# Performance work log

Hardware: AMD Instinct MI355X
Metric: run time of the kernel (lower is better)

The kernel has to match this reference:

```python
import jax, jax.numpy as jnp
import numpy as np

B, NF, S, L, H, MID, KS, NC, DENSE = 16, 8, 16, 256, 128, 32, 8, 10, 512
COEFF = 0.1
BN_EPS = 1e-5


def _normalize(x):
    return x / jnp.maximum(jnp.linalg.norm(x, axis=-1, keepdims=True), 1e-12)


def _sparsemax(z):
    # sparsemax over last axis (Martins & Astudillo 2016)
    zs = jnp.flip(jnp.sort(z, axis=-1), axis=-1)
    k = jnp.arange(1, z.shape[-1] + 1, dtype=z.dtype)
    cum = jnp.cumsum(zs, axis=-1)
    support = (1.0 + k * zs) > cum
    ksup = jnp.sum(support, axis=-1, keepdims=True)
    tau = (jnp.take_along_axis(cum, ksup - 1, axis=-1) - 1.0) / ksup.astype(z.dtype)
    return jnp.maximum(z - tau, 0.0)


def _bn_ncl(x, g, b, m, v):  # eval-mode BatchNorm1d on [N, C, L]
    return g[None, :, None] * (x - m[None, :, None]) * jax.lax.rsqrt(v[None, :, None] + BN_EPS) + b[None, :, None]


def _bn_nc(x, g, b, m, v):  # eval-mode BatchNorm1d on [N, C]
    return g * (x - m) * jax.lax.rsqrt(v + BN_EPS) + b


def _conv(x, w, pad):
    return jax.lax.conv_general_dilated(x, w, (1,), [(pad, pad)], dimension_numbers=('NCH', 'OIH', 'NCH'))


def _maxpool2(x):  # MaxPool1d(kernel=2, stride=2, padding=1): -inf padded
    return jax.lax.reduce_window(x, -jnp.inf, jax.lax.max, (1, 1, 2), (1, 1, 2), ((0, 0), (0, 0), (1, 1)))


def _cnn(x, cw1, bn1, cw2, bn2, cw3, bn3):
    x = _maxpool2(jax.nn.relu(_bn_ncl(_conv(x, cw1, KS // 2), *bn1)))
    x = _maxpool2(jax.nn.relu(_bn_ncl(_conv(x, cw2, 4), *bn2)))
    x = _maxpool2(jax.nn.relu(_bn_ncl(_conv(x, cw3, 4), *bn3)))
    return jnp.mean(x, axis=-1)  # AdaptiveAvgPool1d(1) -> [N, H]


def _alpha_beta(x, cw1, bn1, cw2, bn2, cw3, bn3, Wq, bq, Wk, bk, Wv, bv):
    b = x.shape[0]
    xf = jnp.transpose(x, (1, 0, 2, 3)).reshape(NF, b * S, 1, L)
    rep = jax.vmap(_cnn)(xf, cw1, bn1, cw2, bn2, cw3, bn3)  # [F, B*S, H]
    rep = rep.reshape(NF, b, S, H)
    Q = jax.nn.elu(rep @ Wq + bq)
    K = jax.nn.leaky_relu(rep @ Wk + bk)
    V = jax.nn.leaky_relu(rep @ Wv + bv)
    # mean_t(Q @ K^T) == Q @ mean_t(K); then scale by sqrt(d_k)
    scores = jnp.einsum('fbsh,fbh->fbs', Q, jnp.mean(K, axis=2)) / jnp.sqrt(jnp.float32(H))
    intra_aw = _sparsemax(scores)                             # [F, B, S]
    Z = _normalize(jnp.einsum('fbs,fbsh->fbh', intra_aw, V))  # [F, B, H]
    Kn = _normalize(rep)
    inter_scores = jnp.einsum('ibh,fbsh->ifbs', Z, Kn)        # cosine scores (Z already unit-norm)
    inter_aw = _sparsemax(inter_scores)                       # [I, F, B, S]
    U = jnp.einsum('ifbs,fbsh->ibh', inter_aw, rep) / NF      # mean over feature axis f
    Hc = _normalize(jnp.concatenate([Z, U], axis=-1))         # [F, B, 2H]
    feat = jnp.transpose(Hc, (1, 0, 2)).reshape(b, NF * 2 * H)
    return feat, intra_aw, inter_aw


def _forward(src_x, src_y, tgt_x, cw1, bn1_g, bn1_b, bn1_m, bn1_v, cw2, bn2_g, bn2_b, bn2_m, bn2_v, cw3, bn3_g, bn3_b, bn3_m, bn3_v, Wq, bq, Wk, bk, Wv, bv, bnc1_g, bnc1_b, bnc1_m, bnc1_v, W1, b1, bnc2_g, bnc2_b, bnc2_m, bnc2_v, W2, b2):
    bn1 = (bn1_g, bn1_b, bn1_m, bn1_v)
    bn2 = (bn2_g, bn2_b, bn2_m, bn2_v)
    bn3 = (bn3_g, bn3_b, bn3_m, bn3_v)
    sf, sa, sb = _alpha_beta(src_x, cw1, bn1, cw2, bn2, cw3, bn3, Wq, bq, Wk, bk, Wv, bv)
    _, ta, tb = _alpha_beta(tgt_x, cw1, bn1, cw2, bn2, cw3, bn3, Wq, bq, Wk, bk, Wv, bv)
    h = _bn_nc(sf, bnc1_g, bnc1_b, bnc1_m, bnc1_v) @ W1 + b1
    h = jax.nn.leaky_relu(_bn_nc(h, bnc2_g, bnc2_b, bnc2_m, bnc2_v))
    y_pred = jax.nn.softmax(h @ W2 + b2, axis=-1)
    # MMD domain losses (detached in original via torch.tensor(list))
    da = jnp.mean(sa - ta, axis=-2)                           # [F, S]
    loss_a = COEFF * jnp.mean(jnp.linalg.norm(da, axis=-1))
    db = jnp.mean(sb - tb, axis=-2)                           # [I, F, S]
    loss_b = COEFF * jnp.mean(jnp.sqrt(jnp.sum(db * db, axis=(1, 2))))
    dom = jax.lax.stop_gradient(loss_a + loss_b)
    # CrossEntropyLoss applied to already-softmaxed preds, as in source
    logp = jax.nn.log_softmax(y_pred, axis=-1)
    ce = -jnp.mean(logp[jnp.arange(y_pred.shape[0]), src_y])
    return y_pred, ce + dom


def setup_inputs() -> dict:
    ks = jax.random.split(jax.random.key(0), 40)
    rn = lambda i, sh, s=1.0: s * jax.random.normal(ks[i], sh, dtype=jnp.float32)
    ru = lambda i, sh, lo, hi: jax.random.uniform(ks[i], sh, jnp.float32, lo, hi)
    return {
        'src_x': rn(0, (B, NF, S, L)),
        'src_y': jax.random.randint(ks[1], (B,), 0, NC),
        'tgt_x': rn(2, (B, NF, S, L)),
        'cw1': rn(3, (NF, MID, 1, KS), 0.1),
        'bn1_g': ru(4, (NF, MID), 0.75, 1.25), 'bn1_b': rn(5, (NF, MID), 0.1),
        'bn1_m': rn(6, (NF, MID), 0.1), 'bn1_v': ru(7, (NF, MID), 0.5, 1.5),
        'cw2': rn(8, (NF, 2 * MID, MID, 8), 0.05),
        'bn2_g': ru(9, (NF, 2 * MID), 0.75, 1.25), 'bn2_b': rn(10, (NF, 2 * MID), 0.1),
        'bn2_m': rn(11, (NF, 2 * MID), 0.1), 'bn2_v': ru(12, (NF, 2 * MID), 0.5, 1.5),
        'cw3': rn(13, (NF, H, 2 * MID, 8), 0.05),
        'bn3_g': ru(14, (NF, H), 0.75, 1.25), 'bn3_b': rn(15, (NF, H), 0.1),
        'bn3_m': rn(16, (NF, H), 0.1), 'bn3_v': ru(17, (NF, H), 0.5, 1.5),
        'Wq': rn(18, (H, H), 0.05), 'bq': rn(19, (H,), 0.02),
        'Wk': rn(20, (H, H), 0.05), 'bk': rn(21, (H,), 0.02),
        'Wv': rn(22, (H, H), 0.05), 'bv': rn(23, (H,), 0.02),
        'bnc1_g': ru(24, (NF * 2 * H,), 0.75, 1.25), 'bnc1_b': rn(25, (NF * 2 * H,), 0.1),
        'bnc1_m': rn(26, (NF * 2 * H,), 0.1), 'bnc1_v': ru(27, (NF * 2 * H,), 0.5, 1.5),
        'W1': rn(28, (NF * 2 * H, DENSE), 0.03), 'b1': rn(29, (DENSE,), 0.02),
        'bnc2_g': ru(30, (DENSE,), 0.75, 1.25), 'bnc2_b': rn(31, (DENSE,), 0.1),
        'bnc2_m': rn(32, (DENSE,), 0.1), 'bnc2_v': ru(33, (DENSE,), 0.5, 1.5),
        'W2': rn(34, (DENSE, NC), 0.05), 'b2': rn(35, (NC,), 0.02),
    }


def reference(src_x, src_y, tgt_x, cw1, bn1_g, bn1_b, bn1_m, bn1_v, cw2, bn2_g, bn2_b, bn2_m, bn2_v, cw3, bn3_g, bn3_b, bn3_m, bn3_v, Wq, bq, Wk, bk, Wv, bv, bnc1_g, bnc1_b, bnc1_m, bnc1_v, W1, b1, bnc2_g, bnc2_b, bnc2_m, bnc2_v, W2, b2):
    return _forward(src_x, src_y, tgt_x, cw1, bn1_g, bn1_b, bn1_m, bn1_v, cw2, bn2_g, bn2_b, bn2_m, bn2_v, cw3, bn3_g, bn3_b, bn3_m, bn3_v, Wq, bq, Wk, bk, Wv, bv, bnc1_g, bnc1_b, bnc1_m, bnc1_v, W1, b1, bnc2_g, bnc2_b, bnc2_m, bnc2_v, W2, b2)
```

## Files before the change

kernel.cpp:

```cpp
#include <hip/hip_runtime.h>

typedef unsigned short u16;
typedef unsigned int u32;
typedef __attribute__((ext_vector_type(8))) short bfrag;
typedef __attribute__((ext_vector_type(4))) float ffrag;
typedef __attribute__((ext_vector_type(16))) float ffrag16;

__device__ __forceinline__ float lrelu(float x) { return x >= 0.f ? x : 0.01f * x; }
__device__ __forceinline__ float eluf(float x)  { return x > 0.f ? x : expm1f(x); }
__device__ __forceinline__ u16 f2bf(float f) {
    u32 x = __float_as_uint(f);
    return (u16)((x + 0x7fffu + ((x >> 16) & 1u)) >> 16);
}
__device__ __forceinline__ u16 f2bt(float f) {
    return (u16)(__float_as_uint(f) >> 16);
}
__device__ __forceinline__ float bf2f(u16 u) {
    return __uint_as_float(((u32)u) << 16);
}

__device__ void sparsemax16(const float* z, float* out) {
    float zs[16];
    for (int i = 0; i < 16; ++i) zs[i] = z[i];
    for (int i = 1; i < 16; ++i) {
        float key = zs[i]; int j = i - 1;
        while (j >= 0 && zs[j] < key) { zs[j + 1] = zs[j]; --j; }
        zs[j + 1] = key;
    }
    float cum[16];
    cum[0] = zs[0];
    for (int i = 1; i < 16; ++i) cum[i] = cum[i - 1] + zs[i];
    int ksup = 0;
    for (int k = 1; k <= 16; ++k)
        if (1.0f + (float)k * zs[k - 1] > cum[k - 1]) ksup++;
    if (ksup < 1) ksup = 1;
    float tau = (cum[ksup - 1] - 1.0f) / (float)ksup;
    for (int i = 0; i < 16; ++i) out[i] = fmaxf(z[i] - tau, 0.0f);
}

__global__ __launch_bounds__(256) void k_wprep(
    const float* __restrict__ w2, const float* __restrict__ w3,
    const float* __restrict__ Wq, const float* __restrict__ Wk,
    const float* __restrict__ Wv,
    u16* __restrict__ wpk2, u16* __restrict__ wpk3, u16* __restrict__ wqkv)
{
    int i0 = (blockIdx.x * 256 + threadIdx.x) * 4;
    for (int t = 0; t < 4; ++t) {
        int i = i0 + t;
        if (i < 131072) {
            int j = i & 7, L = (i >> 3) & 63, kc = (i >> 9) & 7, nt = (i >> 12) & 3, f = i >> 14;
            int co = nt * 16 + (L & 15);
            int ci = ((L >> 4) << 3) + j;
            wpk2[i] = f2bf(w2[(((size_t)f * 64 + co) * 32 + ci) * 8 + kc]);
        } else if (i < 131072 + 524288) {
            int i2 = i - 131072;
            int j = i2 & 7, L = (i2 >> 3) & 63, kt = (i2 >> 9) & 31, nt = (i2 >> 14) & 3, f = i2 >> 16;
            int co = nt * 32 + (L & 31);
            int ci = (kt & 3) * 16 + ((L >> 5) << 3) + j;
            int tap = kt >> 2;
            wpk3[i2] = f2bf(w3[(((size_t)f * 128 + co) * 64 + ci) * 8 + tap]);
        } else if (i < 131072 + 524288 + 49152) {
            int j2 = i - 655360;
            int proj = j2 >> 14, idx = j2 & 16383;
            int jj = idx & 7, L = (idx >> 3) & 63, kc = (idx >> 9) & 3, nt = idx >> 11;
            int n = nt * 16 + (L & 15);
            int k = kc * 32 + ((L >> 4) << 3) + jj;
            const float* W = proj == 0 ? Wq : (proj == 1 ? Wk : Wv);
            wqkv[j2] = f2bf(W[k * 128 + n]);
        }
    }
}

#define S1T_STRIDE 40
#define S2T_STRIDE 72
#define RB2_STRIDE 68
#define RB3_STRIDE 140
#define RB_OFF 6336
#define SMEM_U16 (RB_OFF + 67 * RB3_STRIDE)

__global__ __launch_bounds__(256, 3) void k_cnn(
    const float* __restrict__ xs, const float* __restrict__ xt,
    const float* __restrict__ w1, const float* __restrict__ g1, const float* __restrict__ b1,
    const float* __restrict__ m1, const float* __restrict__ v1,
    const float* __restrict__ g2, const float* __restrict__ b2,
    const float* __restrict__ m2, const float* __restrict__ v2,
    const float* __restrict__ g3, const float* __restrict__ b3,
    const float* __restrict__ m3, const float* __restrict__ v3,
    const u16* __restrict__ wpk2, const u16* __restrict__ wpk3,
    float* __restrict__ rep)
{
    __shared__ __align__(16) u16 smem[SMEM_U16];
    float* xin = (float*)(smem + RB_OFF);

    int tid = threadIdx.x, blk = blockIdx.x;
    int pass = blk >> 11, f = (blk >> 8) & 7, n = blk & 255;
    int bb = n >> 4, ss = n & 15;
    int lane = tid & 63, w = tid >> 6;
    const float* x = pass ? xt : xs;
    float* rep_p = rep + (size_t)pass * 262144;

    {
        u32* z = (u32*)smem;
        for (int i = tid; i < 80; i += 256) z[i] = 0;
        for (int i = tid; i < 360; i += 256) z[2660 + i] = 0;
        if (tid < 4) { xin[tid] = 0.f; xin[260 + tid] = 0.f; }
        const float* xr = x + (((size_t)bb * 8 + f) * 16 + ss) * 256;
        for (int i = tid; i < 256; i += 256) xin[i + 4] = xr[i];
    }
    __syncthreads();

    if (tid < 208) {
        int cc = tid & 7, jc = tid >> 3;
        int co0 = cc * 4, j0 = jc * 5;
        float wr[4][8];
        for (int c = 0; c < 4; ++c) {
            const float4* q = reinterpret_cast<const float4*>(w1 + ((size_t)f * 32 + co0 + c) * 8);
            float4 a = q[0], bq = q[1];
            wr[c][0] = a.x; wr[c][1] = a.y; wr[c][2] = a.z; wr[c][3] = a.w;
            wr[c][4] = bq.x; wr[c][5] = bq.y; wr[c][6] = bq.z; wr[c][7] = bq.w;
        }
        int px[10];
        for (int i = 0; i < 10; ++i) {
            int p = 2 * j0 - 1 + i;
            px[i] = p < 0 ? 0 : (p > 256 ? 256 : p);
        }
        float acc[4][10];
        for (int c = 0; c < 4; ++c) for (int i = 0; i < 10; ++i) acc[c][i] = 0.f;
        for (int k = 0; k < 8; ++k) {
            float xv[10];
            for (int i = 0; i < 10; ++i) xv[i] = xin[px[i] + k];
            for (int c = 0; c < 4; ++c)
                for (int i = 0; i < 10; ++i) acc[c][i] += wr[c][k] * xv[i];
        }
        float scv[4], shv[4];
        for (int c = 0; c < 4; ++c) {
            int co = co0 + c;
            scv[c] = g1[f * 32 + co] * rsqrtf(v1[f * 32 + co] + 1e-5f);
            shv[c] = b1[f * 32 + co] - m1[f * 32 + co] * scv[c];
        }
        for (int jj = 0; jj < 5; ++jj) {
            int j = j0 + jj;
            if (j < 129) {
                ushort4 pk;
                {
                    float a0 = fmaxf(acc[0][2*jj] * scv[0] + shv[0], 0.f);
                    float a1 = fmaxf(acc[0][2*jj+1] * scv[0] + shv[0], 0.f);
                    pk.x = f2bt(fmaxf(a0, a1));
                }
                {
                    float a0 = fmaxf(acc[1][2*jj] * scv[1] + shv[1], 0.f);
                    float a1 = fmaxf(acc[1][2*jj+1] * scv[1] + shv[1], 0.f);
                    pk.y = f2bt(fmaxf(a0, a1));
                }
                {
                    float a0 = fmaxf(acc[2][2*jj] * scv[2] + shv[2], 0.f);
                    float a1 = fmaxf(acc[2][2*jj+1] * scv[2] + shv[2], 0.f);
                    pk.z = f2bt(fmaxf(a0, a1));
                }
                {
                    float a0 = fmaxf(acc[3][2*jj] * scv[3] + shv[3], 0.f);
                    float a1 = fmaxf(acc[3][2*jj+1] * scv[3] + shv[3], 0.f);
                    pk.w = f2bt(fmaxf(a0, a1));
                }
                *reinterpret_cast<ushort4*>(&smem[(j + 4) * S1T_STRIDE + co0]) = pk;
            }
        }
    }
    __syncthreads();

    {
        bfrag B2[2][8];
        {
            const bfrag* gB = reinterpret_cast<const bfrag*>(wpk2);
            int wN = w & 1;
#pragma unroll
            for (int t = 0; t < 2; ++t)
#pragma unroll
                for (int kc = 0; kc < 8; ++kc)
                    B2[t][kc] = gB[(((size_t)f * 4 + (wN * 2 + t)) * 8 + kc) * 64 + lane];
        }
        int wM = w >> 1, wN = w & 1;
        float sc2[2], sh2[2];
        int co2[2];
#pragma unroll
        for (int t = 0; t < 2; ++t) {
            int co = (wN * 2 + t) * 16 + (lane & 15);
            co2[t] = co;
            sc2[t] = g2[f * 64 + co] * rsqrtf(v2[f * 64 + co] + 1e-5f);
            sh2[t] = b2[f * 64 + co] - m2[f * 64 + co] * sc2[t];
        }
        int arow = lane & 15, ci0 = (lane >> 4) << 3;
        int mtlo = wM ? 5 : 0, mthi = wM ? 9 : 5;
        for (int mt = mtlo; mt < mthi; ++mt) {
            ffrag C0 = {0.f, 0.f, 0.f, 0.f}, C1 = {0.f, 0.f, 0.f, 0.f};
            int rb = mt * 16 + arow;
#pragma unroll
            for (int kc = 0; kc < 8; ++kc) {
                bfrag A = *reinterpret_cast<const bfrag*>(&smem[(rb + kc) * S1T_STRIDE + ci0]);
                C0 = __builtin_amdgcn_mfma_f32_16x16x32_bf16(A, B2[0][kc], C0, 0, 0, 0);
                C1 = __builtin_amdgcn_mfma_f32_16x16x32_bf16(A, B2[1][kc], C1, 0, 0, 0);
            }
            int p0 = mt * 16 + ((lane >> 4) << 2);
#pragma unroll
            for (int r = 0; r < 4; ++r) {
                int p = p0 + r;
                if (p < 130) {
                    smem[RB_OFF + p * RB2_STRIDE + co2[0]] = f2bt(fmaxf(C0[r] * sc2[0] + sh2[0], 0.f));
                    smem[RB_OFF + p * RB2_STRIDE + co2[1]] = f2bt(fmaxf(C1[r] * sc2[1] + sh2[1], 0.f));
                }
            }
        }
    }
    __syncthreads();

    {
        u32* z = (u32*)smem;
        for (int i = tid; i < 144; i += 256) z[i] = 0;
        for (int i = tid; i < 612; i += 256) z[2520 + i] = 0;
    }
    {
        const u32* rb2 = reinterpret_cast<const u32*>(smem + RB_OFF);
        u32* s2 = reinterpret_cast<u32*>(smem);
        for (int e = tid; e < 66 * 32; e += 256) {
            int j = e >> 5, c2 = e & 31;
            u32 v;
            if (j == 0) {
                v = rb2[c2];
            } else if (j == 65) {
                v = rb2[129 * 34 + c2];
            } else {
                u32 a = rb2[(2 * j - 1) * 34 + c2];
                u32 b = rb2[(2 * j) * 34 + c2];
                float a0 = bf2f((u16)a), a1 = bf2f((u16)(a >> 16));
                float b0 = bf2f((u16)b), b1 = bf2f((u16)(b >> 16));
                u16 m0 = a0 > b0 ? (u16)a : (u16)b;
                u16 m1 = a1 > b1 ? (u16)(a >> 16) : (u16)(b >> 16);
                v = (u32)m0 | ((u32)m1 << 16);
            }
            s2[(j + 4) * 36 + c2] = v;
        }
    }
    __syncthreads();

    {
        int am = lane & 31, hk = (lane >> 5) << 3;
        const bfrag* gB3 = reinterpret_cast<const bfrag*>(wpk3);
        size_t bbase = (((size_t)f * 4 + w) * 32) * 64 + lane;
        ffrag16 C0 = {0.f,0.f,0.f,0.f,0.f,0.f,0.f,0.f,0.f,0.f,0.f,0.f,0.f,0.f,0.f,0.f};
        ffrag16 C1 = {0.f,0.f,0.f,0.f,0.f,0.f,0.f,0.f,0.f,0.f,0.f,0.f,0.f,0.f,0.f,0.f};
        ffrag16 C2 = {0.f,0.f,0.f,0.f,0.f,0.f,0.f,0.f,0.f,0.f,0.f,0.f,0.f,0.f,0.f,0.f};
#pragma unroll 4
        for (int kt = 0; kt < 32; ++kt) {
            int row0 = am + (kt >> 2);
            int ci0 = (kt & 3) * 16 + hk;
            bfrag B = gB3[bbase + (size_t)kt * 64];
            bfrag A0 = *reinterpret_cast<const bfrag*>(&smem[row0 * S2T_STRIDE + ci0]);
            bfrag A1 = *reinterpret_cast<const bfrag*>(&smem[(row0 + 32) * S2T_STRIDE + ci0]);
            bfrag A2 = *reinterpret_cast<const bfrag*>(&smem[(row0 + 64) * S2T_STRIDE + ci0]);
            C0 = __builtin_amdgcn_mfma_f32_32x32x16_bf16(A0, B, C0, 0, 0, 0);
            C1 = __builtin_amdgcn_mfma_f32_32x32x16_bf16(A1, B, C1, 0, 0, 0);
            C2 = __builtin_amdgcn_mfma_f32_32x32x16_bf16(A2, B, C2, 0, 0, 0);
        }
        int ncol = w * 32 + am;
        float sc = g3[f * 128 + ncol] * rsqrtf(v3[f * 128 + ncol] + 1e-5f);
        float sh = b3[f * 128 + ncol] - m3[f * 128 + ncol] * sc;
        int prow_off = (lane >> 5) << 2;
#pragma unroll
        for (int reg = 0; reg < 16; ++reg) {
            int pr = (reg & 3) + 8 * (reg >> 2) + prow_off;
            smem[RB_OFF + pr * RB3_STRIDE + ncol] = f2bt(fmaxf(C0[reg] * sc + sh, 0.f));
            smem[RB_OFF + (32 + pr) * RB3_STRIDE + ncol] = f2bt(fmaxf(C1[reg] * sc + sh, 0.f));
            int p2 = 64 + pr;
            if (p2 < 67)
                smem[RB_OFF + p2 * RB3_STRIDE + ncol] = f2bt(fmaxf(C2[reg] * sc + sh, 0.f));
        }
    }
    __syncthreads();

    if (tid < 128) {
        int co = tid;
        float sum = bf2f(smem[RB_OFF + 0 * RB3_STRIDE + co]);
        for (int j = 1; j < 34; ++j) {
            float a0 = bf2f(smem[RB_OFF + (2 * j - 1) * RB3_STRIDE + co]);
            float a1 = bf2f(smem[RB_OFF + (2 * j) * RB3_STRIDE + co]);
            sum += fmaxf(a0, a1);
        }
        rep_p[(((size_t)f * 256) + n) * 128 + co] = sum * (1.0f / 34.0f);
    }
}

__global__ __launch_bounds__(256) void k_attn1(
    const float* __restrict__ rep, const u16* __restrict__ wqkv,
    const float* __restrict__ bq, const float* __restrict__ bk,
    const float* __restrict__ bv,
    float* __restrict__ Zn, float* __restrict__ rninv, float* __restrict__ iaw)
{
    __shared__ __align__(16) u16 repbf[16 * 136];
    __shared__ float KmL[128], ZL[128], awL[16], scoresL[16], r2L[16];
    __shared__ float spart[4][4][4];
    __shared__ float redL[4];
    int tid = threadIdx.x;
    int pass = blockIdx.x >> 7, f = (blockIdx.x >> 4) & 7, b = blockIdx.x & 15;
    const float* rp = rep + (size_t)pass * 262144 + ((size_t)f * 256 + b * 16) * 128;
    float* Zn_p = Zn + (size_t)pass * 16384;
    float* rninv_p = rninv + (size_t)pass * 2048;
    float* iaw_p = iaw + (size_t)pass * 2048;

    {
        int s = tid >> 4, i = tid & 15, h0 = i * 8;
        const float4* q4 = reinterpret_cast<const float4*>(rp + s * 128 + h0);
        float4 a = q4[0], c = q4[1];
        float p2 = a.x*a.x + a.y*a.y + a.z*a.z + a.w*a.w
                 + c.x*c.x + c.y*c.y + c.z*c.z + c.w*c.w;
        bfrag pk;
        pk[0] = (short)f2bt(a.x); pk[1] = (short)f2bt(a.y);
        pk[2] = (short)f2bt(a.z); pk[3] = (short)f2bt(a.w);
        pk[4] = (short)f2bt(c.x); pk[5] = (short)f2bt(c.y);
        pk[6] = (short)f2bt(c.z); pk[7] = (short)f2bt(c.w);
        *reinterpret_cast<bfrag*>(&repbf[s * 136 + h0]) = pk;
        p2 += __shfl_xor(p2, 1); p2 += __shfl_xor(p2, 2);
        p2 += __shfl_xor(p2, 4); p2 += __shfl_xor(p2, 8);
        if (i == 0) r2L[s] = p2;
    }
    __syncthreads();

    int lane = tid & 63, w = tid >> 6, arow = lane & 15, q = lane >> 4;
    bfrag A[4];
    for (int kc = 0; kc < 4; ++kc)
        A[kc] = *reinterpret_cast<const bfrag*>(&repbf[arow * 136 + kc * 32 + q * 8]);

    float qv[2][4], vvv[2][4];
    int colv[2];
    const bfrag* BB = reinterpret_cast<const bfrag*>(wqkv);
    for (int t = 0; t < 2; ++t) {
        int nt = w * 2 + t;
        ffrag cq = {0.f,0.f,0.f,0.f}, ck = {0.f,0.f,0.f,0.f}, cv = {0.f,0.f,0.f,0.f};
        for (int kc = 0; kc < 4; ++kc) {
            int fi = (nt * 4 + kc) * 64 + lane;
            bfrag Bq = BB[fi];
            bfrag Bk = BB[2048 + fi];
            bfrag Bv = BB[4096 + fi];
            cq = __builtin_amdgcn_mfma_f32_16x16x32_bf16(A[kc], Bq, cq, 0, 0, 0);
            ck = __builtin_amdgcn_mfma_f32_16x16x32_bf16(A[kc], Bk, ck, 0, 0, 0);
            cv = __builtin_amdgcn_mfma_f32_16x16x32_bf16(A[kc], Bv, cv, 0, 0, 0);
        }
        int col = nt * 16 + arow;
        colv[t] = col;
        float bqc = bq[col], bkc = bk[col], bvc = bv[col];
        float kpt = 0.f;
        for (int r = 0; r < 4; ++r) {
            qv[t][r] = eluf(cq[r] + bqc);
            vvv[t][r] = lrelu(cv[r] + bvc);
            kpt += lrelu(ck[r] + bkc);
        }
        kpt += __shfl_xor(kpt, 16);
        kpt += __shfl_xor(kpt, 32);
        if (q == 0) KmL[col] = kpt * (1.f / 16.f);
    }
    __syncthreads();

    {
        float km0 = KmL[colv[0]], km1 = KmL[colv[1]];
        float ps[4];
        for (int r = 0; r < 4; ++r) {
            float v = qv[0][r] * km0 + qv[1][r] * km1;
            v += __shfl_xor(v, 1); v += __shfl_xor(v, 2);
            v += __shfl_xor(v, 4); v += __shfl_xor(v, 8);
            ps[r] = v;
        }
        if (arow == 0)
            for (int r = 0; r < 4; ++r) spart[w][q][r] = ps[r];
    }
    __syncthreads();
    if (tid < 16) {
        int qq = tid >> 2, rr = tid & 3;
        float sc = spart[0][qq][rr] + spart[1][qq][rr] + spart[2][qq][rr] + spart[3][qq][rr];
        scoresL[tid] = sc * 0.08838834764831845f;
        rninv_p[f * 256 + b * 16 + tid] = 1.f / fmaxf(sqrtf(r2L[tid]), 1e-12f);
    }
    __syncthreads();
    if (tid == 0) sparsemax16(scoresL, awL);
    __syncthreads();
    if (tid < 16) iaw_p[f * 256 + b * 16 + tid] = awL[tid];

    for (int t = 0; t < 2; ++t) {
        float zp = 0.f;
        for (int r = 0; r < 4; ++r) zp += awL[q * 4 + r] * vvv[t][r];
        zp += __shfl_xor(zp, 16);
        zp += __shfl_xor(zp, 32);
        if (q == 0) ZL[colv[t]] = zp;
    }
    __syncthreads();
    if (tid < 128) {
        float z = ZL[tid];
        float v = z * z;
        v += __shfl_xor(v, 1); v += __shfl_xor(v, 2); v += __shfl_xor(v, 4);
        v += __shfl_xor(v, 8); v += __shfl_xor(v, 16); v += __shfl_xor(v, 32);
        if (lane == 0) redL[w] = v;
    }
    __syncthreads();
    if (tid == 0) redL[2] = 1.f / fmaxf(sqrtf(redL[0] + redL[1]), 1e-12f);
    __syncthreads();
    if (tid < 128)
        Zn_p[((size_t)f * 16 + b) * 128 + tid] = ZL[tid] * redL[2];
}

__global__ __launch_bounds__(256) void k_attn2(
    const float* __restrict__ rep, const float* __restrict__ Zn,
    const float* __restrict__ rninv, float* __restrict__ ibw,
    const float* __restrict__ g, const float* __restrict__ bb,
    const float* __restrict__ mm, const float* __restrict__ vv,
    float* __restrict__ featbn)
{
    __shared__ float repL[16384];
    __shared__ float ZiL[128], scores[128], UL[128];
    __shared__ float awLf[8][16];
    __shared__ float redL[2];
    int tid = threadIdx.x, blk = blockIdx.x;
    int pass = blk >> 7, b = (blk >> 3) & 15, i = blk & 7;
    const float* rep_p = rep + (size_t)pass * 262144;

    for (int f = 0; f < 8; ++f) {
        const float4* src = reinterpret_cast<const float4*>(
            rep_p + ((size_t)f * 256 + b * 16) * 128);
        float4* dst = reinterpret_cast<float4*>(repL + f * 2048);
        for (int t = tid; t < 512; t += 256) dst[t] = src[t];
    }
    if (tid < 128) ZiL[tid] = Zn[(size_t)pass * 16384 + ((size_t)i * 16 + b) * 128 + tid];
    __syncthreads();

    if (tid < 128) {
        int f = tid >> 4, s = tid & 15;
        const float* rr = repL + tid * 128;
        float a = 0.f;
        for (int h = 0; h < 128; ++h) a += ZiL[h] * rr[h];
        scores[tid] = a * rninv[(size_t)pass * 2048 + f * 256 + b * 16 + s];
    }
    __syncthreads();
    if (tid < 8) {
        float aw[16];
        sparsemax16(&scores[tid * 16], aw);
        for (int s = 0; s < 16; ++s) awLf[tid][s] = aw[s];
    }
    __syncthreads();
    if (tid < 128) {
        int f = tid >> 4, s = tid & 15;
        ibw[(size_t)pass * 16384 + (((size_t)i * 8 + f) * 16 + b) * 16 + s] = awLf[f][s];
    }
    if (pass == 0) {
        if (tid < 128) {
            int h = tid;
            float u = 0.f;
            for (int f = 0; f < 8; ++f) {
                const float* rr = repL + f * 2048 + h;
                const float* aa = awLf[f];
                for (int s = 0; s < 16; ++s) u += aa[s] * rr[s * 128];
            }
            UL[h] = u * 0.125f;
        }
        __syncthreads();
        if (tid < 128) {
            int lane = tid & 63, w = tid >> 6;
            float v = ZiL[tid] * ZiL[tid] + UL[tid] * UL[tid];
            v += __shfl_xor(v, 1); v += __shfl_xor(v, 2); v += __shfl_xor(v, 4);
            v += __shfl_xor(v, 8); v += __shfl_xor(v, 16); v += __shfl_xor(v, 32);
            if (lane == 0) redL[w] = v;
        }
        __syncthreads();
        if (tid < 256) {
            float inv = 1.f / fmaxf(sqrtf(redL[0] + redL[1]), 1e-12f);
            int d = tid;
            int e = i * 256 + d;
            float val = (d < 128 ? ZiL[d] : UL[d - 128]) * inv;
            float scv = g[e] * rsqrtf(vv[e] + 1e-5f);
            featbn[b * 2048 + e] = (val - mm[e]) * scv + bb[e];
        }
    }
}

__global__ __launch_bounds__(256) void k_head1(
    const float* __restrict__ featbn,
    const float* __restrict__ W1, const float* __restrict__ b1,
    const float* __restrict__ g2, const float* __restrict__ bb2,
    const float* __restrict__ mm2, const float* __restrict__ vv2,
    float* __restrict__ h2ws)
{
    __shared__ float featL[2048];
    __shared__ float part[32][32];
    int tid = threadIdx.x, blk = blockIdx.x;
    int b = blk >> 4, cc = blk & 15;
    {
        const float4* src = reinterpret_cast<const float4*>(featbn + b * 2048);
        float4* dst = reinterpret_cast<float4*>(featL);
        for (int i = tid; i < 512; i += 256) dst[i] = src[i];
    }
    __syncthreads();
    int ks = tid >> 3, cg = tid & 7;
    int col0 = cc * 32 + cg * 4;
    float4 acc = {0.f, 0.f, 0.f, 0.f};
    const float* fl = featL + ks * 64;
    for (int c = 0; c < 64; ++c) {
        int k = ks * 64 + c;
        float4 wv = *reinterpret_cast<const float4*>(W1 + (size_t)k * 512 + col0);
        float fv = fl[c];
        acc.x += fv * wv.x; acc.y += fv * wv.y;
        acc.z += fv * wv.z; acc.w += fv * wv.w;
    }
    part[ks][cg * 4 + 0] = acc.x;
    part[ks][cg * 4 + 1] = acc.y;
    part[ks][cg * 4 + 2] = acc.z;
    part[ks][cg * 4 + 3] = acc.w;
    __syncthreads();
    if (tid < 32) {
        int colw = cc * 32 + tid;
        float s = b1[colw];
        for (int k2 = 0; k2 < 32; ++k2) s += part[k2][tid];
        float scv = g2[colw] * rsqrtf(vv2[colw] + 1e-5f);
        float val = (s - mm2[colw]) * scv + bb2[colw];
        h2ws[b * 512 + colw] = lrelu(val);
    }
}

__global__ __launch_bounds__(256) void k_tail(
    const float* __restrict__ h2ws,
    const float* __restrict__ W2, const float* __restrict__ b2,
    const float* __restrict__ sa, const float* __restrict__ ta,
    const float* __restrict__ sb, const float* __restrict__ tb,
    const int* __restrict__ sy, float* __restrict__ dout)
{
    __shared__ float h2L[8192];
    __shared__ float lgL[160], ypL[160];
    __shared__ float sA[8], sB[8];
    int tid = threadIdx.x;
    for (int i = tid; i < 8192; i += 256) h2L[i] = h2ws[i];
    if (tid < 8) { sA[tid] = 0.f; sB[tid] = 0.f; }
    __syncthreads();
    if (tid < 160) {
        int b = tid / 10, j = tid - b * 10;
        float a = b2[j];
        const float* h = h2L + b * 512;
        for (int c = 0; c < 512; ++c) a += h[c] * W2[c * 10 + j];
        lgL[tid] = a;
    }
    __syncthreads();
    if (tid < 16) {
        int b = tid;
        float mx = lgL[b * 10];
        for (int j = 1; j < 10; ++j) mx = fmaxf(mx, lgL[b * 10 + j]);
        float sum = 0.f, ex[10];
        for (int j = 0; j < 10; ++j) { ex[j] = expf(lgL[b * 10 + j] - mx); sum += ex[j]; }
        for (int j = 0; j < 10; ++j) {
            float p = ex[j] / sum;
            ypL[b * 10 + j] = p;
            dout[b * 10 + j] = p;
        }
    }
    __syncthreads();
    if (tid < 128) {
        int f = tid >> 4, s = tid & 15;
        float d = 0.f;
        for (int b = 0; b < 16; ++b) d += sa[f * 256 + b * 16 + s] - ta[f * 256 + b * 16 + s];
        d *= (1.f / 16.f);
        atomicAdd(&sA[f], d * d);
    }
    for (int e = tid; e < 1024; e += 256) {
        int i = e >> 7, f = (e >> 4) & 7, s = e & 15;
        float d = 0.f;
        int base = ((i * 8 + f) * 16) * 16 + s;
        for (int b = 0; b < 16; ++b) d += sb[base + b * 16] - tb[base + b * 16];
        d *= (1.f / 16.f);
        atomicAdd(&sB[i], d * d);
    }
    __syncthreads();
    if (tid == 0) {
        float la = 0.f, lb = 0.f;
        for (int f = 0; f < 8; ++f) la += sqrtf(sA[f]);
        for (int i = 0; i < 8; ++i) lb += sqrtf(sB[i]);
        la *= 0.1f / 8.f;
        lb *= 0.1f / 8.f;
        float ce = 0.f;
        for (int b = 0; b < 16; ++b) {
            const float* y = ypL + b * 10;
            float mx = y[0];
            for (int j = 1; j < 10; ++j) mx = fmaxf(mx, y[j]);
            float sum = 0.f;
            for (int j = 0; j < 10; ++j) sum += expf(y[j] - mx);
            float lse = mx + logf(sum);
            ce += lse - y[sy[b]];
        }
        ce *= (1.f / 16.f);
        dout[160] = ce + la + lb;
    }
}

extern "C" void kernel_launch(void* const* d_in, const int* in_sizes, int n_in,
                              void* d_out, int out_size, void* d_ws, size_t ws_size,
                              hipStream_t stream) {
    (void)in_sizes; (void)n_in; (void)out_size; (void)ws_size;
    const float* src_x = (const float*)d_in[0];
    const int*   src_y = (const int*)d_in[1];
    const float* tgt_x = (const float*)d_in[2];
    const float *cw1 = (const float*)d_in[3], *bn1g = (const float*)d_in[4],
                *bn1b = (const float*)d_in[5], *bn1m = (const float*)d_in[6],
                *bn1v = (const float*)d_in[7];
    const float *cw2 = (const float*)d_in[8], *bn2g = (const float*)d_in[9],
                *bn2b = (const float*)d_in[10], *bn2m = (const float*)d_in[11],
                *bn2v = (const float*)d_in[12];
    const float *cw3 = (const float*)d_in[13], *bn3g = (const float*)d_in[14],
                *bn3b = (const float*)d_in[15], *bn3m = (const float*)d_in[16],
                *bn3v = (const float*)d_in[17];
    const float *Wq = (const float*)d_in[18], *bq = (const float*)d_in[19],
                *Wk = (const float*)d_in[20], *bk = (const float*)d_in[21],
                *Wv = (const float*)d_in[22], *bv = (const float*)d_in[23];
    const float *bc1g = (const float*)d_in[24], *bc1b = (const float*)d_in[25],
                *bc1m = (const float*)d_in[26], *bc1v = (const float*)d_in[27];
    const float *W1 = (const float*)d_in[28], *b1 = (const float*)d_in[29];
    const float *bc2g = (const float*)d_in[30], *bc2b = (const float*)d_in[31],
                *bc2m = (const float*)d_in[32], *bc2v = (const float*)d_in[33];
    const float *W2 = (const float*)d_in[34], *b2 = (const float*)d_in[35];

    float* ws = (float*)d_ws;
    size_t o = 0;
    float* rep    = ws + o; o += (size_t)2 * 262144;
    float* Zn     = ws + o; o += (size_t)2 * 16384;
    float* rninv  = ws + o; o += (size_t)2 * 2048;
    float* ia     = ws + o; o += (size_t)2 * 2048;
    float* ib     = ws + o; o += (size_t)2 * 16384;
    float* featbn = ws + o; o += (size_t)16 * 2048;
    float* h2ws   = ws + o; o += (size_t)16 * 512;
    u16* wpk2 = (u16*)(ws + o); o += 65536;
    u16* wpk3 = (u16*)(ws + o); o += 262144;
    u16* wqkv = (u16*)(ws + o); o += 24576;

    k_wprep<<<688, 256, 0, stream>>>(cw2, cw3, Wq, Wk, Wv, wpk2, wpk3, wqkv);
    k_cnn<<<4096, 256, 0, stream>>>(src_x, tgt_x,
        cw1, bn1g, bn1b, bn1m, bn1v,
        bn2g, bn2b, bn2m, bn2v,
        bn3g, bn3b, bn3m, bn3v,
        wpk2, wpk3, rep);
    k_attn1<<<256, 256, 0, stream>>>(rep, wqkv, bq, bk, bv, Zn, rninv, ia);
    k_attn2<<<256, 256, 0, stream>>>(rep, Zn, rninv, ib, bc1g, bc1b, bc1m, bc1v, featbn);
    k_head1<<<256, 256, 0, stream>>>(featbn, W1, b1, bc2g, bc2b, bc2m, bc2v, h2ws);
    k_tail<<<1, 256, 0, stream>>>(h2ws, W2, b2, ia, ia + 2048, ib, ib + 16384,
                                  src_y, (float*)d_out);
}
```

Baseline: 303.5 us.

## Merge post-CNN attention and head kernels into one cooperative kernel with grid syncs

Replaces the four kernels after the CNN (attn1, attn2, head1, tail) with one cooperative kernel that uses grid.sync() between phases and a shared-memory buffer reused by every phase. The aim is to remove three kernel launch gaps and their inter-kernel drain. In exchange it adds grid-wide barrier costs, leaves all but one block idle during the tail phase, and the large shared-memory footprint could limit co-residency for the cooperative launch.

```diff
diff --git a/kernel.cpp b/kernel.cpp
--- a/kernel.cpp
+++ b/kernel.cpp
@@ -1,4 +1,7 @@
 #include <hip/hip_runtime.h>
+#include <hip/hip_cooperative_groups.h>
+
+namespace cg = cooperative_groups;
 
 typedef unsigned short u16;
 typedef unsigned int u32;
@@ -289,307 +292,321 @@
     }
 }
 
-__global__ __launch_bounds__(256) void k_attn1(
+__global__ __launch_bounds__(256) void k_post(
     const float* __restrict__ rep, const u16* __restrict__ wqkv,
     const float* __restrict__ bq, const float* __restrict__ bk,
     const float* __restrict__ bv,
-    float* __restrict__ Zn, float* __restrict__ rninv, float* __restrict__ iaw)
+    float* __restrict__ Zn, float* __restrict__ rninv,
+    float* __restrict__ ia, float* __restrict__ ib,
+    const float* __restrict__ c1g, const float* __restrict__ c1b,
+    const float* __restrict__ c1m, const float* __restrict__ c1v,
+    float* __restrict__ featbn,
+    const float* __restrict__ W1, const float* __restrict__ b1,
+    const float* __restrict__ c2g, const float* __restrict__ c2b,
+    const float* __restrict__ c2m, const float* __restrict__ c2v,
+    float* __restrict__ h2ws,
+    const float* __restrict__ W2, const float* __restrict__ b2,
+    const int* __restrict__ sy, float* __restrict__ dout)
 {
-    __shared__ __align__(16) u16 repbf[16 * 136];
-    __shared__ float KmL[128], ZL[128], awL[16], scoresL[16], r2L[16];
-    __shared__ float spart[4][4][4];
-    __shared__ float redL[4];
-    int tid = threadIdx.x;
-    int pass = blockIdx.x >> 7, f = (blockIdx.x >> 4) & 7, b = blockIdx.x & 15;
-    const float* rp = rep + (size_t)pass * 262144 + ((size_t)f * 256 + b * 16) * 128;
-    float* Zn_p = Zn + (size_t)pass * 16384;
-    float* rninv_p = rninv + (size_t)pass * 2048;
-    float* iaw_p = iaw + (size_t)pass * 2048;
-
-    {
-        int s = tid >> 4, i = tid & 15, h0 = i * 8;
-        const float4* q4 = reinterpret_cast<const float4*>(rp + s * 128 + h0);
-        float4 a = q4[0], c = q4[1];
-        float p2 = a.x*a.x + a.y*a.y + a.z*a.z + a.w*a.w
-                 + c.x*c.x + c.y*c.y + c.z*c.z + c.w*c.w;
-        bfrag pk;
-        pk[0] = (short)f2bt(a.x); pk[1] = (short)f2bt(a.y);
-        pk[2] = (short)f2bt(a.z); pk[3] = (short)f2bt(a.w);
-        pk[4] = (short)f2bt(c.x); pk[5] = (short)f2bt(c.y);
-        pk[6] = (short)f2bt(c.z); pk[7] = (short)f2bt(c.w);
-        *reinterpret_cast<bfrag*>(&repbf[s * 136 + h0]) = pk;
-        p2 += __shfl_xor(p2, 1); p2 += __shfl_xor(p2, 2);
-        p2 += __shfl_xor(p2, 4); p2 += __shfl_xor(p2, 8);
-        if (i == 0) r2L[s] = p2;
-    }
-    __syncthreads();
-
-    int lane = tid & 63, w = tid >> 6, arow = lane & 15, q = lane >> 4;
-    bfrag A[4];
-    for (int kc = 0; kc < 4; ++kc)
-        A[kc] = *reinterpret_cast<const bfrag*>(&repbf[arow * 136 + kc * 32 + q * 8]);
-
-    float qv[2][4], vvv[2][4];
-    int colv[2];
-    const bfrag* BB = reinterpret_cast<const bfrag*>(wqkv);
-    for (int t = 0; t < 2; ++t) {
-        int nt = w * 2 + t;
-        ffrag cq = {0.f,0.f,0.f,0.f}, ck = {0.f,0.f,0.f,0.f}, cv = {0.f,0.f,0.f,0.f};
-        for (int kc = 0; kc < 4; ++kc) {
-            int fi = (nt * 4 + kc) * 64 + lane;
-            bfrag Bq = BB[fi];
-            bfrag Bk = BB[2048 + fi];
-            bfrag Bv = BB[4096 + fi];
-            cq = __builtin_amdgcn_mfma_f32_16x16x32_bf16(A[kc], Bq, cq, 0, 0, 0);
-            ck = __builtin_amdgcn_mfma_f32_16x16x32_bf16(A[kc], Bk, ck, 0, 0, 0);
-            cv = __builtin_amdgcn_mfma_f32_16x16x32_bf16(A[kc], Bv, cv, 0, 0, 0);
-        }
-        int col = nt * 16 + arow;
-        colv[t] = col;
-        float bqc = bq[col], bkc = bk[col], bvc = bv[col];
-        float kpt = 0.f;
-        for (int r = 0; r < 4; ++r) {
-            qv[t][r] = eluf(cq[r] + bqc);
-            vvv[t][r] = lrelu(cv[r] + bvc);
-            kpt += lrelu(ck[r] + bkc);
-        }
-        kpt += __shfl_xor(kpt, 16);
-        kpt += __shfl_xor(kpt, 32);
-        if (q == 0) KmL[col] = kpt * (1.f / 16.f);
-    }
-    __syncthreads();
-
-    {
-        float km0 = KmL[colv[0]], km1 = KmL[colv[1]];
-        float ps[4];
-        for (int r = 0; r < 4; ++r) {
-            float v = qv[0][r] * km0 + qv[1][r] * km1;
-            v += __shfl_xor(v, 1); v += __shfl_xor(v, 2);
-            v += __shfl_xor(v, 4); v += __shfl_xor(v, 8);
-            ps[r] = v;
-        }
-        if (arow == 0)
-            for (int r = 0; r < 4; ++r) spart[w][q][r] = ps[r];
-    }
-    __syncthreads();
-    if (tid < 16) {
-        int qq = tid >> 2, rr = tid & 3;
-        float sc = spart[0][qq][rr] + spart[1][qq][rr] + spart[2][qq][rr] + spart[3][qq][rr];
-        scoresL[tid] = sc * 0.08838834764831845f;
-        rninv_p[f * 256 + b * 16 + tid] = 1.f / fmaxf(sqrtf(r2L[tid]), 1e-12f);
-    }
-    __syncthreads();
-    if (tid == 0) sparsemax16(scoresL, awL);
-    __syncthreads();
-    if (tid < 16) iaw_p[f * 256 + b * 16 + tid] = awL[tid];
-
-    for (int t = 0; t < 2; ++t) {
-        float zp = 0.f;
-        for (int r = 0; r < 4; ++r) zp += awL[q * 4 + r] * vvv[t][r];
-        zp += __shfl_xor(zp, 16);
-        zp += __shfl_xor(zp, 32);
-        if (q == 0) ZL[colv[t]] = zp;
-    }
-    __syncthreads();
-    if (tid < 128) {
-        float z = ZL[tid];
-        float v = z * z;
-        v += __shfl_xor(v, 1); v += __shfl_xor(v, 2); v += __shfl_xor(v, 4);
-        v += __shfl_xor(v, 8); v += __shfl_xor(v, 16); v += __shfl_xor(v, 32);
-        if (lane == 0) redL[w] = v;
-    }
-    __syncthreads();
-    if (tid == 0) redL[2] = 1.f / fmaxf(sqrtf(redL[0] + redL[1]), 1e-12f);
-    __syncthreads();
-    if (tid < 128)
-        Zn_p[((size_t)f * 16 + b) * 128 + tid] = ZL[tid] * redL[2];
-}
-
-__global__ __launch_bounds__(256) void k_attn2(
-    const float* __restrict__ rep, const float* __restrict__ Zn,
-    const float* __restrict__ rninv, float* __restrict__ ibw,
-    const float* __restrict__ g, const float* __restrict__ bb,
-    const float* __restrict__ mm, const float* __restrict__ vv,
-    float* __restrict__ featbn)
-{
-    __shared__ float repL[16384];
-    __shared__ float ZiL[128], scores[128], UL[128];
-    __shared__ float awLf[8][16];
-    __shared__ float redL[2];
+    cg::grid_group grid = cg::this_grid();
+    __shared__ __align__(16) unsigned char smraw[67712];
     int tid = threadIdx.x, blk = blockIdx.x;
-    int pass = blk >> 7, b = (blk >> 3) & 15, i = blk & 7;
-    const float* rep_p = rep + (size_t)pass * 262144;
-
-    for (int f = 0; f < 8; ++f) {
-        const float4* src = reinterpret_cast<const float4*>(
-            rep_p + ((size_t)f * 256 + b * 16) * 128);
-        float4* dst = reinterpret_cast<float4*>(repL + f * 2048);
-        for (int t = tid; t < 512; t += 256) dst[t] = src[t];
-    }
-    if (tid < 128) ZiL[tid] = Zn[(size_t)pass * 16384 + ((size_t)i * 16 + b) * 128 + tid];
-    __syncthreads();
-
-    if (tid < 128) {
-        int f = tid >> 4, s = tid & 15;
-        const float* rr = repL + tid * 128;
-        float a = 0.f;
-        for (int h = 0; h < 128; ++h) a += ZiL[h] * rr[h];
-        scores[tid] = a * rninv[(size_t)pass * 2048 + f * 256 + b * 16 + s];
-    }
-    __syncthreads();
-    if (tid < 8) {
-        float aw[16];
-        sparsemax16(&scores[tid * 16], aw);
-        for (int s = 0; s < 16; ++s) awLf[tid][s] = aw[s];
-    }
-    __syncthreads();
-    if (tid < 128) {
-        int f = tid >> 4, s = tid & 15;
-        ibw[(size_t)pass * 16384 + (((size_t)i * 8 + f) * 16 + b) * 16 + s] = awLf[f][s];
-    }
-    if (pass == 0) {
+    int lane = tid & 63, w = tid >> 6;
+
+    {
+        u16* repbf = reinterpret_cast<u16*>(smraw);
+        float* KmL = reinterpret_cast<float*>(smraw + 4352);
+        float* ZL = reinterpret_cast<float*>(smraw + 4864);
+        float* awL = reinterpret_cast<float*>(smraw + 5376);
+        float* scoresL = reinterpret_cast<float*>(smraw + 5440);
+        float* r2L = reinterpret_cast<float*>(smraw + 5504);
+        float* spart = reinterpret_cast<float*>(smraw + 5568);
+        float* redL = reinterpret_cast<float*>(smraw + 5824);
+
+        int pass = blk >> 7, f = (blk >> 4) & 7, b = blk & 15;
+        const float* rp = rep + (size_t)pass * 262144 + ((size_t)f * 256 + b * 16) * 128;
+        float* Zn_p = Zn + (size_t)pass * 16384;
+        float* rninv_p = rninv + (size_t)pass * 2048;
+        float* iaw_p = ia + (size_t)pass * 2048;
+
+        {
+            int s = tid >> 4, i = tid & 15, h0 = i * 8;
+            const float4* q4 = reinterpret_cast<const float4*>(rp + s * 128 + h0);
+            float4 a = q4[0], c = q4[1];
+            float p2 = a.x*a.x + a.y*a.y + a.z*a.z + a.w*a.w
+                     + c.x*c.x + c.y*c.y + c.z*c.z + c.w*c.w;
+            bfrag pk;
+            pk[0] = (short)f2bt(a.x); pk[1] = (short)f2bt(a.y);
+            pk[2] = (short)f2bt(a.z); pk[3] = (short)f2bt(a.w);
+            pk[4] = (short)f2bt(c.x); pk[5] = (short)f2bt(c.y);
+            pk[6] = (short)f2bt(c.z); pk[7] = (short)f2bt(c.w);
+            *reinterpret_cast<bfrag*>(&repbf[s * 136 + h0]) = pk;
+            p2 += __shfl_xor(p2, 1); p2 += __shfl_xor(p2, 2);
+            p2 += __shfl_xor(p2, 4); p2 += __shfl_xor(p2, 8);
+            if (i == 0) r2L[s] = p2;
+        }
+        __syncthreads();
+
+        int arow = lane & 15, q = lane >> 4;
+        bfrag A[4];
+        for (int kc = 0; kc < 4; ++kc)
+            A[kc] = *reinterpret_cast<const bfrag*>(&repbf[arow * 136 + kc * 32 + q * 8]);
+
+        float qv[2][4], vvv[2][4];
+        int colv[2];
+        const bfrag* BB = reinterpret_cast<const bfrag*>(wqkv);
+        for (int t = 0; t < 2; ++t) {
+            int nt = w * 2 + t;
+            ffrag cq = {0.f,0.f,0.f,0.f}, ck = {0.f,0.f,0.f,0.f}, cv = {0.f,0.f,0.f,0.f};
+            for (int kc = 0; kc < 4; ++kc) {
+                int fi = (nt * 4 + kc) * 64 + lane;
+                bfrag Bq = BB[fi];
+                bfrag Bk = BB[2048 + fi];
+                bfrag Bv = BB[4096 + fi];
+                cq = __builtin_amdgcn_mfma_f32_16x16x32_bf16(A[kc], Bq, cq, 0, 0, 0);
+                ck = __builtin_amdgcn_mfma_f32_16x16x32_bf16(A[kc], Bk, ck, 0, 0, 0);
+                cv = __builtin_amdgcn_mfma_f32_16x16x32_bf16(A[kc], Bv, cv, 0, 0, 0);
+            }
+            int col = nt * 16 + arow;
+            colv[t] = col;
+            float bqc = bq[col], bkc = bk[col], bvc = bv[col];
+            float kpt = 0.f;
+            for (int r = 0; r < 4; ++r) {
+                qv[t][r] = eluf(cq[r] + bqc);
+                vvv[t][r] = lrelu(cv[r] + bvc);
+                kpt += lrelu(ck[r] + bkc);
+            }
+            kpt += __shfl_xor(kpt, 16);
+            kpt += __shfl_xor(kpt, 32);
+            if (q == 0) KmL[col] = kpt * (1.f / 16.f);
+        }
+        __syncthreads();
+
+        {
+            float km0 = KmL[colv[0]], km1 = KmL[colv[1]];
+            float ps[4];
+            for (int r = 0; r < 4; ++r) {
+                float v = qv[0][r] * km0 + qv[1][r] * km1;
+                v += __shfl_xor(v, 1); v += __shfl_xor(v, 2);
+                v += __shfl_xor(v, 4); v += __shfl_xor(v, 8);
+                ps[r] = v;
+            }
+            if (arow == 0)
+                for (int r = 0; r < 4; ++r) spart[((w << 2) + q) * 4 + r] = ps[r];
+        }
+        __syncthreads();
+        if (tid < 16) {
+            int qq = tid >> 2, rr = tid & 3;
+            float sc = spart[(0 + qq) * 4 + rr] + spart[(4 + qq) * 4 + rr]
+                     + spart[(8 + qq) * 4 + rr] + spart[(12 + qq) * 4 + rr];
+            scoresL[tid] = sc * 0.08838834764831845f;
+            rninv_p[f * 256 + b * 16 + tid] = 1.f / fmaxf(sqrtf(r2L[tid]), 1e-12f);
+        }
+        __syncthreads();
+        if (tid == 0) sparsemax16(scoresL, awL);
+        __syncthreads();
+        if (tid < 16) iaw_p[f * 256 + b * 16 + tid] = awL[tid];
+
+        for (int t = 0; t < 2; ++t) {
+            float zp = 0.f;
+            for (int r = 0; r < 4; ++r) zp += awL[q * 4 + r] * vvv[t][r];
+            zp += __shfl_xor(zp, 16);
+            zp += __shfl_xor(zp, 32);
+            if (q == 0) ZL[colv[t]] = zp;
+        }
+        __syncthreads();
         if (tid < 128) {
-            int h = tid;
-            float u = 0.f;
-            for (int f = 0; f < 8; ++f) {
-                const float* rr = repL + f * 2048 + h;
-                const float* aa = awLf[f];
-                for (int s = 0; s < 16; ++s) u += aa[s] * rr[s * 128];
-            }
-            UL[h] = u * 0.125f;
-        }
-        __syncthreads();
-        if (tid < 128) {
-            int lane = tid & 63, w = tid >> 6;
-            float v = ZiL[tid] * ZiL[tid] + UL[tid] * UL[tid];
+            float z = ZL[tid];
+            float v = z * z;
             v += __shfl_xor(v, 1); v += __shfl_xor(v, 2); v += __shfl_xor(v, 4);
             v += __shfl_xor(v, 8); v += __shfl_xor(v, 16); v += __shfl_xor(v, 32);
             if (lane == 0) redL[w] = v;
         }
         __syncthreads();
-        if (tid < 256) {
-            float inv = 1.f / fmaxf(sqrtf(redL[0] + redL[1]), 1e-12f);
-            int d = tid;
-            int e = i * 256 + d;
-            float val = (d < 128 ? ZiL[d] : UL[d - 128]) * inv;
-            float scv = g[e] * rsqrtf(vv[e] + 1e-5f);
-            featbn[b * 2048 + e] = (val - mm[e]) * scv + bb[e];
-        }
-    }
-}
-
-__global__ __launch_bounds__(256) void k_head1(
-    const float* __restrict__ featbn,
-    const float* __restrict__ W1, const float* __restrict__ b1,
-    const float* __restrict__ g2, const float* __restrict__ bb2,
-    const float* __restrict__ mm2, const float* __restrict__ vv2,
-    float* __restrict__ h2ws)
-{
-    __shared__ float featL[2048];
-    __shared__ float part[32][32];
-    int tid = threadIdx.x, blk = blockIdx.x;
-    int b = blk >> 4, cc = blk & 15;
-    {
-        const float4* src = reinterpret_cast<const float4*>(featbn + b * 2048);
-        float4* dst = reinterpret_cast<float4*>(featL);
-        for (int i = tid; i < 512; i += 256) dst[i] = src[i];
-    }
-    __syncthreads();
-    int ks = tid >> 3, cg = tid & 7;
-    int col0 = cc * 32 + cg * 4;
-    float4 acc = {0.f, 0.f, 0.f, 0.f};
-    const float* fl = featL + ks * 64;
-    for (int c = 0; c < 64; ++c) {
-        int k = ks * 64 + c;
-        float4 wv = *reinterpret_cast<const float4*>(W1 + (size_t)k * 512 + col0);
-        float fv = fl[c];
-        acc.x += fv * wv.x; acc.y += fv * wv.y;
-        acc.z += fv * wv.z; acc.w += fv * wv.w;
-    }
-    part[ks][cg * 4 + 0] = acc.x;
-    part[ks][cg * 4 + 1] = acc.y;
-    part[ks][cg * 4 + 2] = acc.z;
-    part[ks][cg * 4 + 3] = acc.w;
-    __syncthreads();
-    if (tid < 32) {
-        int colw = cc * 32 + tid;
-        float s = b1[colw];
-        for (int k2 = 0; k2 < 32; ++k2) s += part[k2][tid];
-        float scv = g2[colw] * rsqrtf(vv2[colw] + 1e-5f);
-        float val = (s - mm2[colw]) * scv + bb2[colw];
-        h2ws[b * 512 + colw] = lrelu(val);
-    }
-}
-
-__global__ __launch_bounds__(256) void k_tail(
-    const float* __restrict__ h2ws,
-    const float* __restrict__ W2, const float* __restrict__ b2,
-    const float* __restrict__ sa, const float* __restrict__ ta,
-    const float* __restrict__ sb, const float* __restrict__ tb,
-    const int* __restrict__ sy, float* __restrict__ dout)
-{
-    __shared__ float h2L[8192];
-    __shared__ float lgL[160], ypL[160];
-    __shared__ float sA[8], sB[8];
-    int tid = threadIdx.x;
-    for (int i = tid; i < 8192; i += 256) h2L[i] = h2ws[i];
-    if (tid < 8) { sA[tid] = 0.f; sB[tid] = 0.f; }
-    __syncthreads();
-    if (tid < 160) {
-        int b = tid / 10, j = tid - b * 10;
-        float a = b2[j];
-        const float* h = h2L + b * 512;
-        for (int c = 0; c < 512; ++c) a += h[c] * W2[c * 10 + j];
-        lgL[tid] = a;
-    }
-    __syncthreads();
-    if (tid < 16) {
-        int b = tid;
-        float mx = lgL[b * 10];
-        for (int j = 1; j < 10; ++j) mx = fmaxf(mx, lgL[b * 10 + j]);
-        float sum = 0.f, ex[10];
-        for (int j = 0; j < 10; ++j) { ex[j] = expf(lgL[b * 10 + j] - mx); sum += ex[j]; }
-        for (int j = 0; j < 10; ++j) {
-            float p = ex[j] / sum;
-            ypL[b * 10 + j] = p;
-            dout[b * 10 + j] = p;
-        }
-    }
-    __syncthreads();
-    if (tid < 128) {
-        int f = tid >> 4, s = tid & 15;
-        float d = 0.f;
-        for (int b = 0; b < 16; ++b) d += sa[f * 256 + b * 16 + s] - ta[f * 256 + b * 16 + s];
-        d *= (1.f / 16.f);
-        atomicAdd(&sA[f], d * d);
-    }
-    for (int e = tid; e < 1024; e += 256) {
-        int i = e >> 7, f = (e >> 4) & 7, s = e & 15;
-        float d = 0.f;
-        int base = ((i * 8 + f) * 16) * 16 + s;
-        for (int b = 0; b < 16; ++b) d += sb[base + b * 16] - tb[base + b * 16];
-        d *= (1.f / 16.f);
-        atomicAdd(&sB[i], d * d);
-    }
-    __syncthreads();
-    if (tid == 0) {
-        float la = 0.f, lb = 0.f;
-        for (int f = 0; f < 8; ++f) la += sqrtf(sA[f]);
-        for (int i = 0; i < 8; ++i) lb += sqrtf(sB[i]);
-        la *= 0.1f / 8.f;
-        lb *= 0.1f / 8.f;
-        float ce = 0.f;
-        for (int b = 0; b < 16; ++b) {
-            const float* y = ypL + b * 10;
-            float mx = y[0];
-            for (int j = 1; j < 10; ++j) mx = fmaxf(mx, y[j]);
-            float sum = 0.f;
-            for (int j = 0; j < 10; ++j) sum += expf(y[j] - mx);
-            float lse = mx + logf(sum);
-            ce += lse - y[sy[b]];
-        }
-        ce *= (1.f / 16.f);
-        dout[160] = ce + la + lb;
+        if (tid == 0) redL[2] = 1.f / fmaxf(sqrtf(redL[0] + redL[1]), 1e-12f);
+        __syncthreads();
+        if (tid < 128)
+            Zn_p[((size_t)f * 16 + b) * 128 + tid] = ZL[tid] * redL[2];
+    }
+    grid.sync();
+
+    {
+        float* repL = reinterpret_cast<float*>(smraw);
+        float* ZiL = reinterpret_cast<float*>(smraw + 65536);
+        float* scores = reinterpret_cast<float*>(smraw + 66048);
+        float* UL = reinterpret_cast<float*>(smraw + 66560);
+        float* awLf = reinterpret_cast<float*>(smraw + 67072);
+        float* redL = reinterpret_cast<float*>(smraw + 67584);
+
+        int pass = blk >> 7, b = (blk >> 3) & 15, i = blk & 7;
+        const float* rep_p = rep + (size_t)pass * 262144;
+
+        for (int f = 0; f < 8; ++f) {
+            const float4* src = reinterpret_cast<const float4*>(
+                rep_p + ((size_t)f * 256 + b * 16) * 128);
+            float4* dst = reinterpret_cast<float4*>(repL + f * 2048);
+            for (int t = tid; t < 512; t += 256) dst[t] = src[t];
+        }
+        if (tid < 128) ZiL[tid] = Zn[(size_t)pass * 16384 + ((size_t)i * 16 + b) * 128 + tid];
+        __syncthreads();
+
+        if (tid < 128) {
+            int f = tid >> 4, s = tid & 15;
+            const float* rr = repL + tid * 128;
+            float a = 0.f;
+            for (int h = 0; h < 128; ++h) a += ZiL[h] * rr[h];
+            scores[tid] = a * rninv[(size_t)pass * 2048 + f * 256 + b * 16 + s];
+        }
+        __syncthreads();
+        if (tid < 8) {
+            float aw[16];
+            sparsemax16(&scores[tid * 16], aw);
+            for (int s = 0; s < 16; ++s) awLf[tid * 16 + s] = aw[s];
+        }
+        __syncthreads();
+        if (tid < 128) {
+            int f = tid >> 4, s = tid & 15;
+            ib[(size_t)pass * 16384 + (((size_t)i * 8 + f) * 16 + b) * 16 + s] = awLf[f * 16 + s];
+        }
+        if (pass == 0) {
+            if (tid < 128) {
+                int h = tid;
+                float u = 0.f;
+                for (int f = 0; f < 8; ++f) {
+                    const float* rr = repL + f * 2048 + h;
+                    const float* aa = awLf + f * 16;
+                    for (int s = 0; s < 16; ++s) u += aa[s] * rr[s * 128];
+                }
+                UL[h] = u * 0.125f;
+            }
+            __syncthreads();
+            if (tid < 128) {
+                float v = ZiL[tid] * ZiL[tid] + UL[tid] * UL[tid];
+                v += __shfl_xor(v, 1); v += __shfl_xor(v, 2); v += __shfl_xor(v, 4);
+                v += __shfl_xor(v, 8); v += __shfl_xor(v, 16); v += __shfl_xor(v, 32);
+                if (lane == 0) redL[w] = v;
+            }
+            __syncthreads();
+            {
+                float inv = 1.f / fmaxf(sqrtf(redL[0] + redL[1]), 1e-12f);
+                int d = tid;
+                int e = i * 256 + d;
+                float val = (d < 128 ? ZiL[d] : UL[d - 128]) * inv;
+                float scv = c1g[e] * rsqrtf(c1v[e] + 1e-5f);
+                featbn[b * 2048 + e] = (val - c1m[e]) * scv + c1b[e];
+            }
+        }
+    }
+    grid.sync();
+
+    {
+        float* featL = reinterpret_cast<float*>(smraw);
+        float* part = reinterpret_cast<float*>(smraw + 8192);
+
+        int b = blk >> 4, cc = blk & 15;
+        {
+            const float4* src = reinterpret_cast<const float4*>(featbn + b * 2048);
+            float4* dst = reinterpret_cast<float4*>(featL);
+            for (int i = tid; i < 512; i += 256) dst[i] = src[i];
+        }
+        __syncthreads();
+        int ks = tid >> 3, cg2 = tid & 7;
+        int col0 = cc * 32 + cg2 * 4;
+        float4 acc = {0.f, 0.f, 0.f, 0.f};
+        const float* fl = featL + ks * 64;
+        for (int c = 0; c < 64; ++c) {
+            int k = ks * 64 + c;
+            float4 wv = *reinterpret_cast<const float4*>(W1 + (size_t)k * 512 + col0);
+            float fv = fl[c];
+            acc.x += fv * wv.x; acc.y += fv * wv.y;
+            acc.z += fv * wv.z; acc.w += fv * wv.w;
+        }
+        part[ks * 32 + cg2 * 4 + 0] = acc.x;
+        part[ks * 32 + cg2 * 4 + 1] = acc.y;
+        part[ks * 32 + cg2 * 4 + 2] = acc.z;
+        part[ks * 32 + cg2 * 4 + 3] = acc.w;
+        __syncthreads();
+        if (tid < 32) {
+            int colw = cc * 32 + tid;
+            float s = b1[colw];
+            for (int k2 = 0; k2 < 32; ++k2) s += part[k2 * 32 + tid];
+            float scv = c2g[colw] * rsqrtf(c2v[colw] + 1e-5f);
+            float val = (s - c2m[colw]) * scv + c2b[colw];
+            h2ws[b * 512 + colw] = lrelu(val);
+        }
+    }
+    grid.sync();
+
+    if (blk == 0) {
+        float* h2L = reinterpret_cast<float*>(smraw);
+        float* lgL = reinterpret_cast<float*>(smraw + 32768);
+        float* ypL = reinterpret_cast<float*>(smraw + 33408);
+        float* sA = reinterpret_cast<float*>(smraw + 34048);
+        float* sB = reinterpret_cast<float*>(smraw + 34080);
+        const float* sa = ia;
+        const float* ta = ia + 2048;
+        const float* sb = ib;
+        const float* tb = ib + 16384;
+
+        for (int i = tid; i < 8192; i += 256) h2L[i] = h2ws[i];
+        if (tid < 8) { sA[tid] = 0.f; sB[tid] = 0.f; }
+        __syncthreads();
+        if (tid < 160) {
+            int b = tid / 10, j = tid - b * 10;
+            float a = b2[j];
+            const float* h = h2L + b * 512;
+            for (int c = 0; c < 512; ++c) a += h[c] * W2[c * 10 + j];
+            lgL[tid] = a;
+        }
+        __syncthreads();
+        if (tid < 16) {
+            int b = tid;
+            float mx = lgL[b * 10];
+            for (int j = 1; j < 10; ++j) mx = fmaxf(mx, lgL[b * 10 + j]);
+            float sum = 0.f, ex[10];
+            for (int j = 0; j < 10; ++j) { ex[j] = expf(lgL[b * 10 + j] - mx); sum += ex[j]; }
+            for (int j = 0; j < 10; ++j) {
+                float p = ex[j] / sum;
+                ypL[b * 10 + j] = p;
+                dout[b * 10 + j] = p;
+            }
+        }
+        __syncthreads();
+        if (tid < 128) {
+            int f = tid >> 4, s = tid & 15;
+            float d = 0.f;
+            for (int b = 0; b < 16; ++b) d += sa[f * 256 + b * 16 + s] - ta[f * 256 + b * 16 + s];
+            d *= (1.f / 16.f);
+            atomicAdd(&sA[f], d * d);
+        }
+        for (int e = tid; e < 1024; e += 256) {
+            int i = e >> 7, f = (e >> 4) & 7, s = e & 15;
+            float d = 0.f;
+            int base = ((i * 8 + f) * 16) * 16 + s;
+            for (int b = 0; b < 16; ++b) d += sb[base + b * 16] - tb[base + b * 16];
+            d *= (1.f / 16.f);
+            atomicAdd(&sB[i], d * d);
+        }
+        __syncthreads();
+        if (tid == 0) {
+            float la = 0.f, lb = 0.f;
+            for (int f = 0; f < 8; ++f) la += sqrtf(sA[f]);
+            for (int i = 0; i < 8; ++i) lb += sqrtf(sB[i]);
+            la *= 0.1f / 8.f;
+            lb *= 0.1f / 8.f;
+            float ce = 0.f;
+            for (int b = 0; b < 16; ++b) {
+                const float* y = ypL + b * 10;
+                float mx = y[0];
+                for (int j = 1; j < 10; ++j) mx = fmaxf(mx, y[j]);
+                float sum = 0.f;
+                for (int j = 0; j < 10; ++j) sum += expf(y[j] - mx);
+                float lse = mx + logf(sum);
+                ce += lse - y[sy[b]];
+            }
+            ce *= (1.f / 16.f);
+            dout[160] = ce + la + lb;
+        }
     }
 }
 
@@ -638,9 +655,16 @@
         bn2g, bn2b, bn2m, bn2v,
         bn3g, bn3b, bn3m, bn3v,
         wpk2, wpk3, rep);
-    k_attn1<<<256, 256, 0, stream>>>(rep, wqkv, bq, bk, bv, Zn, rninv, ia);
-    k_attn2<<<256, 256, 0, stream>>>(rep, Zn, rninv, ib, bc1g, bc1b, bc1m, bc1v, featbn);
-    k_head1<<<256, 256, 0, stream>>>(featbn, W1, b1, bc2g, bc2b, bc2m, bc2v, h2ws);
-    k_tail<<<1, 256, 0, stream>>>(h2ws, W2, b2, ia, ia + 2048, ib, ib + 16384,
-                                  src_y, (float*)d_out);
-}
+
+    float* dout_f = (float*)d_out;
+    void* args[] = {
+        (void*)&rep, (void*)&wqkv, (void*)&bq, (void*)&bk, (void*)&bv,
+        (void*)&Zn, (void*)&rninv, (void*)&ia, (void*)&ib,
+        (void*)&bc1g, (void*)&bc1b, (void*)&bc1m, (void*)&bc1v,
+        (void*)&featbn,
+        (void*)&W1, (void*)&b1, (void*)&bc2g, (void*)&bc2b, (void*)&bc2m, (void*)&bc2v,
+        (void*)&h2ws,
+        (void*)&W2, (void*)&b2, (void*)&src_y, (void*)&dout_f };
+    hipLaunchCooperativeKernel((const void*)k_post, dim3(256), dim3(256),
+                               args, 0, stream);
+}
```

New measurement: 429.7 us. +41.6%, slower.
